# Kernel tuning notes

Hardware: AMD Instinct MI355X
Metric: run time of the kernel (lower is better)

## Reference

```python
import jax, jax.numpy as jnp
import numpy as np

EMB = 256
IN_CH = 256
CTX_D = 128


def setup_inputs() -> dict:
    key = jax.random.key(0)
    ks = jax.random.split(key, 12)
    b, c, h, w = 16, IN_CH, 48, 48
    seq = 2048
    s = 0.02
    return {
        "x": jax.random.normal(ks[0], (b, c, h, w), jnp.float32),
        "context": jax.random.normal(ks[1], (b, seq, CTX_D), jnp.float32),
        "pad_mask": jax.random.bernoulli(ks[2], 0.1, (b, h * w, seq)),
        "W_in": jax.random.normal(ks[3], (EMB, IN_CH), jnp.float32) * s,   # 1x1 conv weight
        "b_in": jnp.zeros((EMB,), jnp.float32),
        "Wq": jax.random.normal(ks[4], (EMB, EMB), jnp.float32) * s,
        "bq": jnp.zeros((EMB,), jnp.float32),
        "Wk": jax.random.normal(ks[5], (EMB, CTX_D), jnp.float32) * s,
        "bk": jnp.zeros((EMB,), jnp.float32),
        "Wv": jax.random.normal(ks[6], (EMB, CTX_D), jnp.float32) * s,
        "bv": jnp.zeros((EMB,), jnp.float32),
        "W_out": jax.random.normal(ks[7], (IN_CH, EMB), jnp.float32) * s,  # 1x1 conv weight
        "b_out": jnp.zeros((IN_CH,), jnp.float32),
    }


def reference(x, context, pad_mask, W_in, b_in, Wq, bq, Wk, bk, Wv, bv, W_out, b_out):
    b, c, h, w = x.shape
    scale = EMB ** (-0.5)
    # proj_in: 1x1 conv == channel matmul; then b c h w -> b (h w) c
    xt = jnp.einsum('bchw,ec->behw', x, W_in) + b_in[None, :, None, None]
    xt = xt.reshape(b, EMB, h * w).transpose(0, 2, 1)          # [b, hw, emb]
    Q = xt @ Wq.T + bq                                          # [b, hw, emb]
    K = context @ Wk.T + bk                                     # [b, seq, emb]
    V = context @ Wv.T + bv                                     # [b, seq, emb]
    att = jnp.einsum('bid,bjd->bij', Q, K) * scale              # [b, hw, seq]
    att = jnp.where(pad_mask, jnp.float32(-1e9), att)
    att = jax.nn.softmax(att, axis=-1)
    out = jnp.einsum('bij,bjd->bid', att, V)                    # [b, hw, emb]
    out = out.transpose(0, 2, 1).reshape(b, EMB, h, w)
    out = jnp.einsum('behw,ce->bchw', out, W_out) + b_out[None, :, None, None]
    return out, att
```

## Files before the change

### kernel.cpp

```cpp
#include <hip/hip_runtime.h>

typedef unsigned short u16;
typedef unsigned int   u32;
typedef __attribute__((ext_vector_type(8))) __bf16 bf16x8;
typedef __attribute__((ext_vector_type(4))) float  f32x4;

#define BB   16
#define CH   256
#define HW   2304
#define SEQ  2048
#define EMB  256
#define CTXD 128
#define OUT0 9437184

#define MFMA(a,b,c) __builtin_amdgcn_mfma_f32_16x16x32_bf16(a,b,c,0,0,0)

__device__ __forceinline__ u16 f2bf(float f){
  u32 u = __builtin_bit_cast(u32, f);
  u += 0x7fffu + ((u >> 16) & 1u);
  return (u16)(u >> 16);
}
__device__ __forceinline__ float bf2f(u32 us){ return __builtin_bit_cast(float, us << 16); }

__device__ __forceinline__ bf16x8 ld16(const u16* p){
  uint4 q = *reinterpret_cast<const uint4*>(p);
  return __builtin_bit_cast(bf16x8, q);
}
__device__ __forceinline__ bf16x8 ld16c(const char* p){
  uint4 q = *reinterpret_cast<const uint4*>(p);
  return __builtin_bit_cast(bf16x8, q);
}
__device__ __forceinline__ bf16x8 mk8(float a0,float a1,float a2,float a3,
                                      float a4,float a5,float a6,float a7){
  uint4 q;
  q.x = (u32)f2bf(a0) | ((u32)f2bf(a1) << 16);
  q.y = (u32)f2bf(a2) | ((u32)f2bf(a3) << 16);
  q.z = (u32)f2bf(a4) | ((u32)f2bf(a5) << 16);
  q.w = (u32)f2bf(a6) | ((u32)f2bf(a7) << 16);
  return __builtin_bit_cast(bf16x8, q);
}
__device__ __forceinline__ void gload16(const u16* g, u16* l){
  __builtin_amdgcn_global_load_lds(
      (const __attribute__((address_space(1))) unsigned int*)(const void*)g,
      (__attribute__((address_space(3))) unsigned int*)(void*)l, 16, 0, 0);
}

__global__ __launch_bounds__(256) void k_prep(
    const float* __restrict__ Wq, const float* __restrict__ W_in,
    const float* __restrict__ b_in, const float* __restrict__ bq,
    const float* __restrict__ Wk, const float* __restrict__ Wv,
    const float* __restrict__ Wout,
    u16* __restrict__ WqinBf, u16* __restrict__ WkBf, u16* __restrict__ WvBf,
    u16* __restrict__ WoutBf, float* __restrict__ bq_eff)
{
  int blk = blockIdx.x, t = threadIdx.x;
  const float SC = 0.0625f;
  if (blk < 256) {
    int e = blk, c = t;
    float s = 0.f;
    #pragma unroll 8
    for (int f = 0; f < 256; f++) s += Wq[e*256+f] * W_in[f*256+c];
    WqinBf[e*256+c] = f2bf(s * SC);
    __shared__ float rb[4];
    float pb = Wq[e*256+t] * b_in[t];
    pb += __shfl_xor(pb, 1);  pb += __shfl_xor(pb, 2);
    pb += __shfl_xor(pb, 4);  pb += __shfl_xor(pb, 8);
    pb += __shfl_xor(pb, 16); pb += __shfl_xor(pb, 32);
    if ((t & 63) == 0) rb[t >> 6] = pb;
    __syncthreads();
    if (t == 0) bq_eff[e] = (rb[0]+rb[1]+rb[2]+rb[3] + bq[e]) * SC;
  } else {
    u32 flat = (u32)(blk - 256) * 256 + t;
    for (u32 idx = flat; idx < 131072u; idx += 16384u) {
      if (idx < 32768u)       WkBf[idx]          = f2bf(Wk[idx]);
      else if (idx < 65536u)  WvBf[idx - 32768u] = f2bf(Wv[idx - 32768u]);
      else                    WoutBf[idx - 65536u] = f2bf(Wout[idx - 65536u]);
    }
  }
}

__global__ __launch_bounds__(256) void k_qproj(
    const float* __restrict__ x, const u16* __restrict__ WqinBf,
    const float* __restrict__ bq_eff, u16* __restrict__ Qbf)
{
  int b = blockIdx.y, ibase = blockIdx.x * 64;
  int t = threadIdx.x, wv = t >> 6, lane = t & 63, g4 = lane >> 4, r16 = lane & 15;
  int e0 = wv * 64;
  f32x4 acc[4][4] = {};
  #pragma unroll 2
  for (int kk = 0; kk < 8; kk++) {
    bf16x8 a[4];
    #pragma unroll
    for (int m = 0; m < 4; m++)
      a[m] = ld16(WqinBf + (size_t)(e0 + m*16 + r16) * 256 + kk*32 + g4*8);
    bf16x8 bb[4];
    #pragma unroll
    for (int n = 0; n < 4; n++) {
      const float* xp = x + ((size_t)b*CH + kk*32 + g4*8) * HW + ibase + n*16 + r16;
      bb[n] = mk8(xp[0], xp[HW], xp[2*HW], xp[3*HW], xp[4*HW], xp[5*HW], xp[6*HW], xp[7*HW]);
    }
    #pragma unroll
    for (int m = 0; m < 4; m++)
      #pragma unroll
      for (int n = 0; n < 4; n++)
        acc[m][n] = MFMA(a[m], bb[n], acc[m][n]);
  }
  #pragma unroll
  for (int m = 0; m < 4; m++) {
    int e = e0 + m*16 + g4*4;
    float b0 = bq_eff[e], b1 = bq_eff[e+1], b2 = bq_eff[e+2], b3 = bq_eff[e+3];
    #pragma unroll
    for (int n = 0; n < 4; n++) {
      int i = ibase + n*16 + r16;
      u32 lo = (u32)f2bf(acc[m][n][0] + b0) | ((u32)f2bf(acc[m][n][1] + b1) << 16);
      u32 hi = (u32)f2bf(acc[m][n][2] + b2) | ((u32)f2bf(acc[m][n][3] + b3) << 16);
      *(uint2*)(Qbf + ((size_t)b*HW + i) * EMB + e) = make_uint2(lo, hi);
    }
  }
}

__global__ __launch_bounds__(512) void k_kvproj(
    const float* __restrict__ ctx, const u16* __restrict__ WkBf, const u16* __restrict__ WvBf,
    const float* __restrict__ bk, const float* __restrict__ bv,
    u16* __restrict__ Kbf, u16* __restrict__ Vtb)
{
  int b = blockIdx.y, sbase = blockIdx.x * 64;
  int t = threadIdx.x, wv = t >> 6, lane = t & 63, g4 = lane >> 4, r16 = lane & 15;
  bool isV = wv >= 4;
  int e0 = (wv & 3) * 64;
  const u16* Wsel = isV ? WvBf : WkBf;
  f32x4 acc[4][4] = {};
  #pragma unroll
  for (int kk = 0; kk < 4; kk++) {
    bf16x8 a[4];
    #pragma unroll
    for (int m = 0; m < 4; m++)
      a[m] = ld16(Wsel + (size_t)(e0 + m*16 + r16) * 128 + kk*32 + g4*8);
    bf16x8 bb[4];
    #pragma unroll
    for (int n = 0; n < 4; n++) {
      const float* cp = ctx + ((size_t)b*SEQ + sbase + n*16 + r16) * CTXD + kk*32 + g4*8;
      float4 lo = *(const float4*)cp;
      float4 hi = *(const float4*)(cp + 4);
      bb[n] = mk8(lo.x, lo.y, lo.z, lo.w, hi.x, hi.y, hi.z, hi.w);
    }
    #pragma unroll
    for (int m = 0; m < 4; m++)
      #pragma unroll
      for (int n = 0; n < 4; n++)
        acc[m][n] = MFMA(a[m], bb[n], acc[m][n]);
  }
  if (!isV) {
    #pragma unroll
    for (int m = 0; m < 4; m++) {
      int e = e0 + m*16 + g4*4;
      float b0 = bk[e], b1 = bk[e+1], b2 = bk[e+2], b3 = bk[e+3];
      #pragma unroll
      for (int n = 0; n < 4; n++) {
        int s = sbase + n*16 + r16;
        u32 lo = (u32)f2bf(acc[m][n][0] + b0) | ((u32)f2bf(acc[m][n][1] + b1) << 16);
        u32 hi = (u32)f2bf(acc[m][n][2] + b2) | ((u32)f2bf(acc[m][n][3] + b3) << 16);
        *(uint2*)(Kbf + ((size_t)b*SEQ + s) * EMB + e) = make_uint2(lo, hi);
      }
    }
  } else {
    #pragma unroll
    for (int m = 0; m < 4; m++) {
      #pragma unroll
      for (int r = 0; r < 4; r++) {
        int e = e0 + m*16 + g4*4 + r;
        float bvv = bv[e];
        #pragma unroll
        for (int n = 0; n < 4; n++) {
          int s = sbase + n*16 + r16;
          Vtb[((size_t)b*EMB + e) * SEQ + s] = f2bf(acc[m][n][r] + bvv);
        }
      }
    }
  }
}

__global__ __launch_bounds__(512, 4) void k_qk(
    const u16* __restrict__ Qbf, const u16* __restrict__ Kbf,
    const int* __restrict__ mask, float* __restrict__ dout,
    float* __restrict__ gpart)
{
  __shared__ u16 lsA[128*64];
  __shared__ u16 lsB[128*64];
  __shared__ float red[4][128];

  int bid = blockIdx.x;
  int work = (bid & 7) * 576 + (bid >> 3);
  int b = work / 288, rem = work % 288;
  int mt = rem / 16, jt = rem % 16;
  int mbase = mt * 128, jbase = jt * 128;
  size_t bH = (size_t)b * HW, bS = (size_t)b * SEQ;

  int t = threadIdx.x, lane = t & 63, wv = t >> 6, g4 = lane >> 4, r16 = lane & 15;
  int wr = wv >> 2, wc = wv & 3;

  int mreg[4][2][4];
  {
    const int* mp = mask + (bH + mbase + wr*64 + g4*4) * SEQ + jbase + wc*32 + r16;
    #pragma unroll
    for (int m = 0; m < 4; m++)
      #pragma unroll
      for (int n = 0; n < 2; n++)
        #pragma unroll
        for (int r = 0; r < 4; r++)
          mreg[m][n][r] = mp[(size_t)(m*16 + r) * SEQ + n*16];
  }

  int i0 = t, i1 = t + 512;
  int r0 = i0 >> 3, c0 = (i0 & 7) ^ (r0 & 7);
  int r1 = i1 >> 3, c1 = (i1 & 7) ^ (r1 & 7);
  const u16* qs0 = Qbf + (bH + mbase + r0) * 256 + c0*8;
  const u16* qs1 = Qbf + (bH + mbase + r1) * 256 + c1*8;
  const u16* ks0 = Kbf + (bS + jbase + r0) * 256 + c0*8;
  const u16* ks1 = Kbf + (bS + jbase + r1) * 256 + c1*8;
  u16 *dA0 = lsA + i0*8, *dA1 = lsA + i1*8, *dB0 = lsB + i0*8, *dB1 = lsB + i1*8;

  const char* lA = (const char*)lsA;
  const char* lB = (const char*)lsB;

  f32x4 acc[4][2] = {};
  #pragma unroll 1
  for (int ks = 0; ks < 4; ks++) {
    gload16(qs0 + ks*64, dA0);
    gload16(qs1 + ks*64, dA1);
    gload16(ks0 + ks*64, dB0);
    gload16(ks1 + ks*64, dB1);
    __syncthreads();
    #pragma unroll
    for (int kk = 0; kk < 2; kk++) {
      bf16x8 af[4], bf[2];
      #pragma unroll
      for (int m = 0; m < 4; m++) {
        int row = wr*64 + m*16 + r16;
        af[m] = ld16c(lA + row*128 + (((kk<<2)|g4) ^ (row&7))*16);
      }
      #pragma unroll
      for (int n = 0; n < 2; n++) {
        int row = wc*32 + n*16 + r16;
        bf[n] = ld16c(lB + row*128 + (((kk<<2)|g4) ^ (row&7))*16);
      }
      #pragma unroll
      for (int m = 0; m < 4; m++)
        #pragma unroll
        for (int n = 0; n < 2; n++)
          acc[m][n] = MFMA(af[m], bf[n], acc[m][n]);
    }
    __syncthreads();
  }

  u16* Ebase = (u16*)(dout + OUT0);
  float part[4][4] = {};
  #pragma unroll
  for (int m = 0; m < 4; m++)
    #pragma unroll
    for (int n = 0; n < 2; n++)
      #pragma unroll
      for (int r = 0; r < 4; r++) {
        float e = mreg[m][n][r] ? 0.f : __expf(acc[m][n][r]);
        part[m][r] += e;
        int i = wr*64 + m*16 + g4*4 + r;
        int j = jbase + wc*32 + n*16 + r16;
        Ebase[(bH + mbase + i) * 4096 + 2048 + j] = f2bf(e);
      }
  #pragma unroll
  for (int m = 0; m < 4; m++)
    #pragma unroll
    for (int r = 0; r < 4; r++) {
      float v = part[m][r];
      v += __shfl_xor(v, 1); v += __shfl_xor(v, 2);
      v += __shfl_xor(v, 4); v += __shfl_xor(v, 8);
      if (r16 == 0) red[wc][wr*64 + m*16 + g4*4 + r] = v;
    }
  __syncthreads();
  if (t < 128) {
    float tot = red[0][t] + red[1][t] + red[2][t] + red[3][t];
    gpart[(bH + mbase + t) * 16 + jt] = tot;
  }
}

__global__ __launch_bounds__(256) void k_inv(
    const float* __restrict__ gpart, float* __restrict__ invrs)
{
  int row = blockIdx.x * 256 + threadIdx.x;
  const float4* pp = (const float4*)(gpart + (size_t)row * 16);
  float4 p0 = pp[0], p1 = pp[1], p2 = pp[2], p3 = pp[3];
  invrs[row] = 1.f / (p0.x+p0.y+p0.z+p0.w + p1.x+p1.y+p1.z+p1.w
                    + p2.x+p2.y+p2.z+p2.w + p3.x+p3.y+p3.z+p3.w);
}

__global__ __launch_bounds__(256, 3) void k_pv(
    const u16* __restrict__ Vtb, const float* __restrict__ invrs,
    const float* __restrict__ dout, u16* __restrict__ Obf)
{
  __shared__ u16 lsA[128*64];
  __shared__ u16 lsB[128*64];

  int bid = blockIdx.x;
  int work = (bid & 7) * 72 + (bid >> 3);
  int b = work / 36, rem = work % 36;
  int mt = rem >> 1, nt = rem & 1;
  int mbase = mt * 128, ebase = nt * 128;
  size_t bH = (size_t)b * HW;

  int t = threadIdx.x, lane = t & 63, wv = t >> 6, g4 = lane >> 4, r16 = lane & 15;
  int wr = wv >> 1, wc = wv & 1;

  const u16* Ebase = (const u16*)(dout + OUT0);
  int rs[4], cs[4];
  #pragma unroll
  for (int q = 0; q < 4; q++) {
    int idx = q*256 + t;
    rs[q] = idx >> 3;
    cs[q] = (idx & 7) ^ (rs[q] & 7);
  }
  const char* lA = (const char*)lsA;
  const char* lB = (const char*)lsB;

  f32x4 acc[4][4] = {};
  #pragma unroll 1
  for (int ks = 0; ks < 32; ks++) {
    int kb = ks * 64;
    #pragma unroll
    for (int q = 0; q < 4; q++) {
      gload16(Ebase + (bH + mbase + rs[q]) * 4096 + 2048 + kb + cs[q]*8,
              lsA + (q*256 + t)*8);
      gload16(Vtb + ((size_t)b*EMB + ebase + rs[q]) * SEQ + kb + cs[q]*8,
              lsB + (q*256 + t)*8);
    }
    __syncthreads();
    #pragma unroll
    for (int kk = 0; kk < 2; kk++) {
      bf16x8 af[4], bf[4];
      #pragma unroll
      for (int m = 0; m < 4; m++) {
        int row = wr*64 + m*16 + r16;
        af[m] = ld16c(lA + row*128 + (((kk<<2)|g4) ^ (row&7))*16);
      }
      #pragma unroll
      for (int n = 0; n < 4; n++) {
        int row = wc*64 + n*16 + r16;
        bf[n] = ld16c(lB + row*128 + (((kk<<2)|g4) ^ (row&7))*16);
      }
      #pragma unroll
      for (int m = 0; m < 4; m++)
        #pragma unroll
        for (int n = 0; n < 4; n++)
          acc[m][n] = MFMA(af[m], bf[n], acc[m][n]);
    }
    __syncthreads();
  }

  #pragma unroll
  for (int m = 0; m < 4; m++)
    #pragma unroll
    for (int r = 0; r < 4; r++) {
      int i = wr*64 + m*16 + g4*4 + r;
      float iv = invrs[bH + mbase + i];
      #pragma unroll
      for (int n = 0; n < 4; n++) {
        int e = ebase + wc*64 + n*16 + r16;
        Obf[(bH + mbase + i) * 256 + e] = f2bf(acc[m][n][r] * iv);
      }
    }
}

__global__ __launch_bounds__(512, 4) void k_att(
    const float* __restrict__ invrs, float* __restrict__ dout)
{
  int bid = blockIdx.x;
  int work = (bid & 7) * 288 + (bid >> 3);
  int t = threadIdx.x, wv = t >> 6, lane = t & 63;

  #pragma unroll
  for (int rr = 0; rr < 2; rr++) {
    size_t row = (size_t)work * 16 + wv * 2 + rr;
    const u16* Erow = (const u16*)(dout + OUT0) + row * 4096 + 2048;
    float* arow = dout + OUT0 + row * 2048;
    float iv = invrs[row];
    uint2 raw[8];
    #pragma unroll
    for (int seg = 0; seg < 8; seg++)
      raw[seg] = *(const uint2*)(Erow + (size_t)(seg*64 + lane) * 4);
    asm volatile("s_waitcnt vmcnt(0)" ::: "memory");
    #pragma unroll
    for (int seg = 0; seg < 8; seg++) {
      float4 o;
      o.x = bf2f(raw[seg].x & 0xffffu) * iv;
      o.y = bf2f(raw[seg].x >> 16)     * iv;
      o.z = bf2f(raw[seg].y & 0xffffu) * iv;
      o.w = bf2f(raw[seg].y >> 16)     * iv;
      *(float4*)(arow + (size_t)(seg*64 + lane) * 4) = o;
    }
  }
}

__global__ __launch_bounds__(256) void k_outproj(
    const u16* __restrict__ Obf, const u16* __restrict__ WoutBf,
    const float* __restrict__ bout, float* __restrict__ out)
{
  int b = blockIdx.y, ibase = blockIdx.x * 64;
  int t = threadIdx.x, wv = t >> 6, lane = t & 63, g4 = lane >> 4, r16 = lane & 15;
  int c0 = wv * 64;
  f32x4 acc[4][4] = {};
  #pragma unroll 2
  for (int kk = 0; kk < 8; kk++) {
    bf16x8 a[4];
    #pragma unroll
    for (int m = 0; m < 4; m++)
      a[m] = ld16(WoutBf + (size_t)(c0 + m*16 + r16) * 256 + kk*32 + g4*8);
    bf16x8 bb[4];
    #pragma unroll
    for (int n = 0; n < 4; n++)
      bb[n] = ld16(Obf + ((size_t)b*HW + ibase + n*16 + r16) * EMB + kk*32 + g4*8);
    #pragma unroll
    for (int m = 0; m < 4; m++)
      #pragma unroll
      for (int n = 0; n < 4; n++)
        acc[m][n] = MFMA(a[m], bb[n], acc[m][n]);
  }
  #pragma unroll
  for (int m = 0; m < 4; m++) {
    #pragma unroll
    for (int r = 0; r < 4; r++) {
      int c = c0 + m*16 + g4*4 + r;
      float bo = bout[c];
      #pragma unroll
      for (int n = 0; n < 4; n++) {
        int i = ibase + n*16 + r16;
        out[((size_t)b*CH + c) * HW + i] = acc[m][n][r] + bo;
      }
    }
  }
}

extern "C" void kernel_launch(void* const* d_in, const int* in_sizes, int n_in,
                              void* d_out, int out_size, void* d_ws, size_t ws_size,
                              hipStream_t stream)
{
  const float* x    = (const float*)d_in[0];
  const float* ctx  = (const float*)d_in[1];
  const int*   mask = (const int*)  d_in[2];
  const float* W_in = (const float*)d_in[3];
  const float* b_in = (const float*)d_in[4];
  const float* Wq   = (const float*)d_in[5];
  const float* bq   = (const float*)d_in[6];
  const float* Wk   = (const float*)d_in[7];
  const float* bk   = (const float*)d_in[8];
  const float* Wv   = (const float*)d_in[9];
  const float* bv   = (const float*)d_in[10];
  const float* Wout = (const float*)d_in[11];
  const float* bout = (const float*)d_in[12];
  float* out = (float*)d_out;

  char* ws = (char*)d_ws;
  size_t off = 0;
  auto alloc = [&](size_t bytes) -> void* {
    void* p = ws + off;
    off += (bytes + 255) & ~(size_t)255;
    return p;
  };
  u16*   WqinBf = (u16*)  alloc(256*256*2);
  u16*   WkBf   = (u16*)  alloc(256*128*2);
  u16*   WvBf   = (u16*)  alloc(256*128*2);
  u16*   WoutBf = (u16*)  alloc(256*256*2);
  float* bq_eff = (float*)alloc(256*4);
  float* gpart  = (float*)alloc((size_t)BB*HW*16*4);
  float* invrs  = (float*)alloc((size_t)BB*HW*4);
  u16*   Qbf    = (u16*)  alloc((size_t)BB*HW*EMB*2);
  u16*   Kbf    = (u16*)  alloc((size_t)BB*SEQ*EMB*2);
  u16*   Vtb    = (u16*)  alloc((size_t)BB*EMB*SEQ*2);
  if (off > ws_size) return;

  k_prep<<<dim3(320), dim3(256), 0, stream>>>(Wq, W_in, b_in, bq, Wk, Wv, Wout,
                                              WqinBf, WkBf, WvBf, WoutBf, bq_eff);
  k_qproj<<<dim3(36, 16), dim3(256), 0, stream>>>(x, WqinBf, bq_eff, Qbf);
  k_kvproj<<<dim3(32, 16), dim3(512), 0, stream>>>(ctx, WkBf, WvBf, bk, bv, Kbf, Vtb);
  k_qk<<<dim3(4608), dim3(512), 0, stream>>>(Qbf, Kbf, mask, out, gpart);
  k_inv<<<dim3(144), dim3(256), 0, stream>>>(gpart, invrs);
  k_pv<<<dim3(576), dim3(256), 0, stream>>>(Vtb, invrs, out, Qbf );
  k_att<<<dim3(2304), dim3(512), 0, stream>>>(invrs, out);
  k_outproj<<<dim3(36, 16), dim3(256), 0, stream>>>(Qbf , WoutBf, bout, out);
}
```

Measured before the change: 410.6 us.

## Stage exp tile through LDS for coalesced stores and fold k_inv into consumers

The QK kernel now writes its bf16 exp values into shared memory first and then copies them out to global memory as 16-byte row-contiguous stores, replacing scattered 2-byte stores. The separate inverse-row-sum kernel is removed. k_pv now computes the reciprocals for its 128 rows from the partial sums into shared memory, and k_att reduces the 16 partials per row with wave shuffles. This saves a kernel launch and strided global writes, at the cost of some redundant reduction work and extra LDS traffic. It relies on the LDS tiles being free after the main loop's final sync, and k_pv reads invl after the k-loop's __syncthreads.

Result: no change. 417.0 us (+1.6%).

```diff
diff --git a/kernel.cpp b/kernel.cpp
--- a/kernel.cpp
+++ b/kernel.cpp
@@ -253,7 +253,6 @@
     __syncthreads();
   }
 
-  u16* Ebase = (u16*)(dout + OUT0);
   float part[4][4] = {};
   #pragma unroll
   for (int m = 0; m < 4; m++)
@@ -264,8 +263,9 @@
         float e = mreg[m][n][r] ? 0.f : __expf(acc[m][n][r]);
         part[m][r] += e;
         int i = wr*64 + m*16 + g4*4 + r;
-        int j = jbase + wc*32 + n*16 + r16;
-        Ebase[(bH + mbase + i) * 4096 + 2048 + j] = f2bf(e);
+        int jl = wc*32 + n*16 + r16;
+        u16* dst = (i < 64) ? lsA : lsB;
+        dst[(i & 63)*128 + jl] = f2bf(e);
       }
   #pragma unroll
   for (int m = 0; m < 4; m++)
@@ -281,24 +281,25 @@
     float tot = red[0][t] + red[1][t] + red[2][t] + red[3][t];
     gpart[(bH + mbase + t) * 16 + jt] = tot;
   }
-}
-
-__global__ __launch_bounds__(256) void k_inv(
-    const float* __restrict__ gpart, float* __restrict__ invrs)
-{
-  int row = blockIdx.x * 256 + threadIdx.x;
-  const float4* pp = (const float4*)(gpart + (size_t)row * 16);
-  float4 p0 = pp[0], p1 = pp[1], p2 = pp[2], p3 = pp[3];
-  invrs[row] = 1.f / (p0.x+p0.y+p0.z+p0.w + p1.x+p1.y+p1.z+p1.w
-                    + p2.x+p2.y+p2.z+p2.w + p3.x+p3.y+p3.z+p3.w);
+  u16* Ebase = (u16*)(dout + OUT0);
+  #pragma unroll
+  for (int q = 0; q < 4; q++) {
+    int s = q*512 + t;
+    int i = s >> 4;
+    int seg = (s & 15) * 8;
+    const u16* src = ((i < 64) ? lsA : lsB) + (i & 63)*128 + seg;
+    uint4 v = *(const uint4*)src;
+    *(uint4*)(Ebase + (bH + mbase + i) * 4096 + 2048 + jbase + seg) = v;
+  }
 }
 
 __global__ __launch_bounds__(256, 3) void k_pv(
-    const u16* __restrict__ Vtb, const float* __restrict__ invrs,
+    const u16* __restrict__ Vtb, const float* __restrict__ gpart,
     const float* __restrict__ dout, u16* __restrict__ Obf)
 {
   __shared__ u16 lsA[128*64];
   __shared__ u16 lsB[128*64];
+  __shared__ float invl[128];
 
   int bid = blockIdx.x;
   int work = (bid & 7) * 72 + (bid >> 3);
@@ -310,6 +311,13 @@
   int t = threadIdx.x, lane = t & 63, wv = t >> 6, g4 = lane >> 4, r16 = lane & 15;
   int wr = wv >> 1, wc = wv & 1;
 
+  if (t < 128) {
+    const float4* pp = (const float4*)(gpart + (bH + mbase + t) * 16);
+    float4 p0 = pp[0], p1 = pp[1], p2 = pp[2], p3 = pp[3];
+    invl[t] = 1.f / (p0.x+p0.y+p0.z+p0.w + p1.x+p1.y+p1.z+p1.w
+                   + p2.x+p2.y+p2.z+p2.w + p3.x+p3.y+p3.z+p3.w);
+  }
+
   const u16* Ebase = (const u16*)(dout + OUT0);
   int rs[4], cs[4];
   #pragma unroll
@@ -360,7 +368,7 @@
     #pragma unroll
     for (int r = 0; r < 4; r++) {
       int i = wr*64 + m*16 + g4*4 + r;
-      float iv = invrs[bH + mbase + i];
+      float iv = invl[i];
       #pragma unroll
       for (int n = 0; n < 4; n++) {
         int e = ebase + wc*64 + n*16 + r16;
@@ -370,7 +378,7 @@
 }
 
 __global__ __launch_bounds__(512, 4) void k_att(
-    const float* __restrict__ invrs, float* __restrict__ dout)
+    const float* __restrict__ gpart, float* __restrict__ dout)
 {
   int bid = blockIdx.x;
   int work = (bid & 7) * 288 + (bid >> 3);
@@ -381,7 +389,10 @@
     size_t row = (size_t)work * 16 + wv * 2 + rr;
     const u16* Erow = (const u16*)(dout + OUT0) + row * 4096 + 2048;
     float* arow = dout + OUT0 + row * 2048;
-    float iv = invrs[row];
+    float v = gpart[row * 16 + (lane & 15)];
+    v += __shfl_xor(v, 1); v += __shfl_xor(v, 2);
+    v += __shfl_xor(v, 4); v += __shfl_xor(v, 8);
+    float iv = 1.f / v;
     uint2 raw[8];
     #pragma unroll
     for (int seg = 0; seg < 8; seg++)
@@ -470,7 +481,6 @@
   u16*   WoutBf = (u16*)  alloc(256*256*2);
   float* bq_eff = (float*)alloc(256*4);
   float* gpart  = (float*)alloc((size_t)BB*HW*16*4);
-  float* invrs  = (float*)alloc((size_t)BB*HW*4);
   u16*   Qbf    = (u16*)  alloc((size_t)BB*HW*EMB*2);
   u16*   Kbf    = (u16*)  alloc((size_t)BB*SEQ*EMB*2);
   u16*   Vtb    = (u16*)  alloc((size_t)BB*EMB*SEQ*2);
@@ -481,8 +491,7 @@
   k_qproj<<<dim3(36, 16), dim3(256), 0, stream>>>(x, WqinBf, bq_eff, Qbf);
   k_kvproj<<<dim3(32, 16), dim3(512), 0, stream>>>(ctx, WkBf, WvBf, bk, bv, Kbf, Vtb);
   k_qk<<<dim3(4608), dim3(512), 0, stream>>>(Qbf, Kbf, mask, out, gpart);
-  k_inv<<<dim3(144), dim3(256), 0, stream>>>(gpart, invrs);
-  k_pv<<<dim3(576), dim3(256), 0, stream>>>(Vtb, invrs, out, Qbf );
-  k_att<<<dim3(2304), dim3(512), 0, stream>>>(invrs, out);
+  k_pv<<<dim3(576), dim3(256), 0, stream>>>(Vtb, gpart, out, Qbf );
+  k_att<<<dim3(2304), dim3(512), 0, stream>>>(gpart, out);
   k_outproj<<<dim3(36, 16), dim3(256), 0, stream>>>(Qbf , WoutBf, bout, out);
 }
```

## Fuse softmax-inverse and attention normalization into PV kernel with full-EMB tiles

Applied to the files above, without the earlier changes.

Removes the separate k_inv and k_att kernels. k_pv now computes the per-row inverse softmax sums from gpart into shared memory, then after the PV GEMM rewrites its own attention rows in place as normalized fp32. The PV tiling changes from 128x128 (M x EMB) to 64x256, so each block covers the whole embedding. The unnormalized bf16 attention tile is therefore loaded once instead of twice, and the later attention pass finds it recently touched in cache. The trade-off is more LDS per block and a serial 16-row normalization tail inside each block, which may lower occupancy.

Result: slower. 426.8 us (+3.9%).

```diff
diff --git a/kernel.cpp b/kernel.cpp
--- a/kernel.cpp
+++ b/kernel.cpp
@@ -283,68 +283,68 @@
   }
 }
 
-__global__ __launch_bounds__(256) void k_inv(
-    const float* __restrict__ gpart, float* __restrict__ invrs)
-{
-  int row = blockIdx.x * 256 + threadIdx.x;
-  const float4* pp = (const float4*)(gpart + (size_t)row * 16);
-  float4 p0 = pp[0], p1 = pp[1], p2 = pp[2], p3 = pp[3];
-  invrs[row] = 1.f / (p0.x+p0.y+p0.z+p0.w + p1.x+p1.y+p1.z+p1.w
-                    + p2.x+p2.y+p2.z+p2.w + p3.x+p3.y+p3.z+p3.w);
-}
-
 __global__ __launch_bounds__(256, 3) void k_pv(
-    const u16* __restrict__ Vtb, const float* __restrict__ invrs,
-    const float* __restrict__ dout, u16* __restrict__ Obf)
-{
-  __shared__ u16 lsA[128*64];
-  __shared__ u16 lsB[128*64];
+    const u16* __restrict__ Vtb, const float* __restrict__ gpart,
+    float* __restrict__ dout, u16* __restrict__ Obf)
+{
+  __shared__ u16 lsE[64*64];
+  __shared__ u16 lsV[256*64];
+  __shared__ float invl[64];
 
   int bid = blockIdx.x;
   int work = (bid & 7) * 72 + (bid >> 3);
-  int b = work / 36, rem = work % 36;
-  int mt = rem >> 1, nt = rem & 1;
-  int mbase = mt * 128, ebase = nt * 128;
+  int b = work / 36, mt = work % 36;
+  int mbase = mt * 64;
   size_t bH = (size_t)b * HW;
 
   int t = threadIdx.x, lane = t & 63, wv = t >> 6, g4 = lane >> 4, r16 = lane & 15;
-  int wr = wv >> 1, wc = wv & 1;
+
+  if (t < 64) {
+    const float4* pp = (const float4*)(gpart + (bH + mbase + t) * 16);
+    float4 p0 = pp[0], p1 = pp[1], p2 = pp[2], p3 = pp[3];
+    invl[t] = 1.f / (p0.x+p0.y+p0.z+p0.w + p1.x+p1.y+p1.z+p1.w
+                   + p2.x+p2.y+p2.z+p2.w + p3.x+p3.y+p3.z+p3.w);
+  }
 
   const u16* Ebase = (const u16*)(dout + OUT0);
-  int rs[4], cs[4];
-  #pragma unroll
-  for (int q = 0; q < 4; q++) {
-    int idx = q*256 + t;
-    rs[q] = idx >> 3;
-    cs[q] = (idx & 7) ^ (rs[q] & 7);
-  }
-  const char* lA = (const char*)lsA;
-  const char* lB = (const char*)lsB;
+  int sE1 = t + 256;
+  int rE0 = t >> 3,   cE0 = (t & 7)   ^ (rE0 & 7);
+  int rE1 = sE1 >> 3, cE1 = (sE1 & 7) ^ (rE1 & 7);
+  const u16* ep0 = Ebase + (bH + mbase + rE0) * 4096 + 2048 + cE0*8;
+  const u16* ep1 = Ebase + (bH + mbase + rE1) * 4096 + 2048 + cE1*8;
+  int rV[8], cV[8];
+  #pragma unroll
+  for (int i = 0; i < 8; i++) {
+    int idx = i*256 + t;
+    rV[i] = idx >> 3;
+    cV[i] = (idx & 7) ^ (rV[i] & 7);
+  }
+  const u16* Vb = Vtb + (size_t)b * EMB * SEQ;
+  const char* lE = (const char*)lsE;
+  const char* lV = (const char*)lsV;
 
   f32x4 acc[4][4] = {};
   #pragma unroll 1
   for (int ks = 0; ks < 32; ks++) {
     int kb = ks * 64;
-    #pragma unroll
-    for (int q = 0; q < 4; q++) {
-      gload16(Ebase + (bH + mbase + rs[q]) * 4096 + 2048 + kb + cs[q]*8,
-              lsA + (q*256 + t)*8);
-      gload16(Vtb + ((size_t)b*EMB + ebase + rs[q]) * SEQ + kb + cs[q]*8,
-              lsB + (q*256 + t)*8);
-    }
+    gload16(ep0 + kb, lsE + t*8);
+    gload16(ep1 + kb, lsE + sE1*8);
+    #pragma unroll
+    for (int i = 0; i < 8; i++)
+      gload16(Vb + (size_t)rV[i] * SEQ + kb + cV[i]*8, lsV + (i*256 + t)*8);
     __syncthreads();
     #pragma unroll
     for (int kk = 0; kk < 2; kk++) {
       bf16x8 af[4], bf[4];
       #pragma unroll
       for (int m = 0; m < 4; m++) {
-        int row = wr*64 + m*16 + r16;
-        af[m] = ld16c(lA + row*128 + (((kk<<2)|g4) ^ (row&7))*16);
+        int row = m*16 + r16;
+        af[m] = ld16c(lE + row*128 + (((kk<<2)|g4) ^ (row&7))*16);
       }
       #pragma unroll
       for (int n = 0; n < 4; n++) {
-        int row = wc*64 + n*16 + r16;
-        bf[n] = ld16c(lB + row*128 + (((kk<<2)|g4) ^ (row&7))*16);
+        int row = wv*64 + n*16 + r16;
+        bf[n] = ld16c(lV + row*128 + (((kk<<2)|g4) ^ (row&7))*16);
       }
       #pragma unroll
       for (int m = 0; m < 4; m++)
@@ -359,29 +359,22 @@
   for (int m = 0; m < 4; m++)
     #pragma unroll
     for (int r = 0; r < 4; r++) {
-      int i = wr*64 + m*16 + g4*4 + r;
-      float iv = invrs[bH + mbase + i];
+      int i = m*16 + g4*4 + r;
+      float iv = invl[i];
       #pragma unroll
       for (int n = 0; n < 4; n++) {
-        int e = ebase + wc*64 + n*16 + r16;
+        int e = wv*64 + n*16 + r16;
         Obf[(bH + mbase + i) * 256 + e] = f2bf(acc[m][n][r] * iv);
       }
     }
-}
-
-__global__ __launch_bounds__(512, 4) void k_att(
-    const float* __restrict__ invrs, float* __restrict__ dout)
-{
-  int bid = blockIdx.x;
-  int work = (bid & 7) * 288 + (bid >> 3);
-  int t = threadIdx.x, wv = t >> 6, lane = t & 63;
-
-  #pragma unroll
-  for (int rr = 0; rr < 2; rr++) {
-    size_t row = (size_t)work * 16 + wv * 2 + rr;
-    const u16* Erow = (const u16*)(dout + OUT0) + row * 4096 + 2048;
+
+  #pragma unroll 1
+  for (int rr = 0; rr < 16; rr++) {
+    int i = rr*4 + wv;
+    size_t row = bH + mbase + i;
+    const u16* Erow = Ebase + row * 4096 + 2048;
     float* arow = dout + OUT0 + row * 2048;
-    float iv = invrs[row];
+    float iv = invl[i];
     uint2 raw[8];
     #pragma unroll
     for (int seg = 0; seg < 8; seg++)
@@ -470,7 +463,6 @@
   u16*   WoutBf = (u16*)  alloc(256*256*2);
   float* bq_eff = (float*)alloc(256*4);
   float* gpart  = (float*)alloc((size_t)BB*HW*16*4);
-  float* invrs  = (float*)alloc((size_t)BB*HW*4);
   u16*   Qbf    = (u16*)  alloc((size_t)BB*HW*EMB*2);
   u16*   Kbf    = (u16*)  alloc((size_t)BB*SEQ*EMB*2);
   u16*   Vtb    = (u16*)  alloc((size_t)BB*EMB*SEQ*2);
@@ -481,8 +473,6 @@
   k_qproj<<<dim3(36, 16), dim3(256), 0, stream>>>(x, WqinBf, bq_eff, Qbf);
   k_kvproj<<<dim3(32, 16), dim3(512), 0, stream>>>(ctx, WkBf, WvBf, bk, bv, Kbf, Vtb);
   k_qk<<<dim3(4608), dim3(512), 0, stream>>>(Qbf, Kbf, mask, out, gpart);
-  k_inv<<<dim3(144), dim3(256), 0, stream>>>(gpart, invrs);
-  k_pv<<<dim3(576), dim3(256), 0, stream>>>(Vtb, invrs, out, Qbf );
-  k_att<<<dim3(2304), dim3(512), 0, stream>>>(invrs, out);
+  k_pv<<<dim3(576), dim3(256), 0, stream>>>(Vtb, gpart, out, Qbf );
   k_outproj<<<dim3(36, 16), dim3(256), 0, stream>>>(Qbf , WoutBf, bout, out);
 }
```
